# Kernel optimization log

Measured on AMD Instinct MI355X. Metric: run time of the kernel, lower is better.

The kernel has to match this reference:

```python
import jax, jax.numpy as jnp
import numpy as np

K_SEM = 5          # max_semantic_edges
THRESH = 0.2       # semantic_threshold
NEG_INF = -1e30


def setup_inputs() -> dict:
    key = jax.random.key(0)
    k1, k2 = jax.random.split(key)
    message_embeddings = jax.random.normal(k1, (8192, 256), dtype=jnp.float32)
    edge_emb_table = jax.random.normal(k2, (2, 64), dtype=jnp.float32)
    return {"message_embeddings": message_embeddings, "edge_emb_table": edge_emb_table}


def reference(message_embeddings, edge_emb_table):
    N = message_embeddings.shape[0]

    # ---- temporal edges: for each i -> [i,i+1] then [i+1,i] (interleaved) ----
    i = jnp.arange(N - 1)
    fwd = jnp.stack([i, i + 1])            # [2, N-1]
    bwd = jnp.stack([i + 1, i])            # [2, N-1]
    temporal = jnp.stack([fwd, bwd], axis=2).reshape(2, -1)   # [2, 2(N-1)]
    n_temporal = 2 * (N - 1)

    # ---- semantic edges: per-row top-k over sim[i, :i] with threshold ----
    norm = jnp.sqrt(jnp.sum(message_embeddings * message_embeddings, axis=1, keepdims=True))
    emb_n = message_embeddings / jnp.maximum(norm, 1e-12)     # F.normalize(p=2)
    sim = emb_n @ emb_n.T                                      # [N, N]

    r = jnp.arange(N)[:, None]
    c = jnp.arange(N)[None, :]
    # zero out diagonal and adjacent (temporal) pairs, as the torch mask does
    sim = sim * (jnp.abs(r - c) > 1)
    # restrict candidates to j < i (strictly earlier messages)
    cand = jnp.where(c < r, sim, NEG_INF)                      # [N, N]

    vals, idxs = jax.lax.top_k(cand, K_SEM)                    # [N, K]
    sem_src = idxs.reshape(-1)                                 # [N*K]
    sem_dst = jnp.repeat(jnp.arange(N), K_SEM)                 # [N*K]
    sem_valid = (vals > THRESH).reshape(-1)                    # [N*K]

    # ---- assemble padded fixed-size edge set ----
    edge_index = jnp.concatenate([temporal, jnp.stack([sem_src, sem_dst])], axis=1)
    edge_types = jnp.concatenate(
        [jnp.zeros((n_temporal,), jnp.int32), jnp.ones((N * K_SEM,), jnp.int32)])
    valid = jnp.concatenate([jnp.ones((n_temporal,), bool), sem_valid])

    edge_attr = edge_emb_table[edge_types] * valid[:, None].astype(edge_emb_table.dtype)
    edge_index = jnp.where(valid[None, :], edge_index, -1)
    return edge_index, edge_attr, valid
```

## Files before the change

kernel.cpp:

```cpp
#include <hip/hip_runtime.h>

#define N_MSG 8192
#define DIM 256
#define KS 5
#define THRESH 0.2f
#define QSCALE 192.0f
#define FILT_I 6672
#define N_TEMPORAL (2*(N_MSG-1))
#define N_EDGES (N_TEMPORAL + N_MSG*KS)
#define ATTR_OFF (2*N_EDGES)
#define VALID_OFF (ATTR_OFF + N_EDGES*64)
#define BM 128
#define NTILE (N_MSG / BM)
#define NBLOCKS (NTILE*(NTILE+1)/2)
#define CAP 32

typedef int   i32x4 __attribute__((ext_vector_type(4)));

__device__ __forceinline__ void gload_lds16(const void* g, void* l) {
    __builtin_amdgcn_global_load_lds(
        (const __attribute__((address_space(1))) void*)g,
        (__attribute__((address_space(3))) void*)l, 16, 0, 0);
}

__device__ __forceinline__ void ins5(float v, int j, float (&vv)[KS], int (&xx)[KS]) {
    float cv = v; int cj = j;
#pragma unroll
    for (int k = 0; k < KS; ++k) {
        bool b = (cv > vv[k]) || (cv == vv[k] && cj < xx[k]);
        float tv = b ? vv[k] : cv; int tj = b ? xx[k] : cj;
        vv[k] = b ? cv : vv[k];    xx[k] = b ? cj : xx[k];
        cv = tv; cj = tj;
    }
}

__global__ void normalize_k(const float* __restrict__ emb, float* __restrict__ embn,
                            unsigned int* __restrict__ embq, int* __restrict__ cnt) {
    int lane = threadIdx.x & 63;
    int row = blockIdx.x * 4 + (threadIdx.x >> 6);
    const float4 x = *(const float4*)(emb + (size_t)row * DIM + lane * 4);
    float ss = x.x * x.x;
    ss = fmaf(x.y, x.y, ss); ss = fmaf(x.z, x.z, ss); ss = fmaf(x.w, x.w, ss);
#pragma unroll
    for (int off = 1; off <= 32; off <<= 1) ss += __shfl_xor(ss, off);
    float nrm = fmaxf(sqrtf(ss), 1e-12f);
    float4 y; y.x = x.x / nrm; y.y = x.y / nrm; y.z = x.z / nrm; y.w = x.w / nrm;
    *(float4*)(embn + (size_t)row * DIM + lane * 4) = y;
    int q0 = (int)rintf(fminf(fmaxf(y.x * QSCALE, -127.f), 127.f));
    int q1 = (int)rintf(fminf(fmaxf(y.y * QSCALE, -127.f), 127.f));
    int q2 = (int)rintf(fminf(fmaxf(y.z * QSCALE, -127.f), 127.f));
    int q3 = (int)rintf(fminf(fmaxf(y.w * QSCALE, -127.f), 127.f));
    embq[(size_t)row * 64 + lane] =
        (q0 & 255) | ((q1 & 255) << 8) | ((q2 & 255) << 16) | ((q3 & 255) << 24);
    if (lane == 0) cnt[row] = 0;
}

__global__ __launch_bounds__(256, 4)
void sim_filter_k(const signed char* __restrict__ embq, int* __restrict__ cnt,
                  int* __restrict__ cidx) {
    __shared__ __align__(16) signed char Aq[2][BM * 64];
    __shared__ __align__(16) signed char Bq[2][BM * 64];

    int t = blockIdx.x;
    int bi = (int)((sqrtf(8.0f * (float)t + 1.0f) - 1.0f) * 0.5f);
    while ((bi + 1) * (bi + 2) / 2 <= t) ++bi;
    while (bi * (bi + 1) / 2 > t) --bi;
    int bj = t - bi * (bi + 1) / 2;
    const int i0 = bi * BM, j0 = bj * BM;

    const int tid = threadIdx.x;
    const int lane = tid & 63;
    const int ws = tid >> 6;
    const int wm = ws >> 1, wn = ws & 1;
    const int lr = lane & 15, kb = lane >> 4;

    const int gm = tid & 127;
    const int gk1 = tid >> 7, gk2 = gk1 + 2;

    const signed char* rowA = embq + (size_t)(i0 + gm) * DIM;
    const signed char* rowB = embq + (size_t)(j0 + gm) * DIM;

    auto stage = [&](int step, int buf) {
        gload_lds16(rowA + step * 64 + gk1 * 16, &Aq[buf][(size_t)tid * 16]);
        gload_lds16(rowA + step * 64 + gk2 * 16, &Aq[buf][((size_t)tid + 256) * 16]);
        gload_lds16(rowB + step * 64 + gk1 * 16, &Bq[buf][(size_t)tid * 16]);
        gload_lds16(rowB + step * 64 + gk2 * 16, &Bq[buf][((size_t)tid + 256) * 16]);
        asm volatile("" ::: "memory");
    };

    i32x4 acc[4][4];
#pragma unroll
    for (int m = 0; m < 4; ++m)
#pragma unroll
        for (int n = 0; n < 4; ++n) { i32x4 z = {0, 0, 0, 0}; acc[m][n] = z; }

    auto compute = [&](int slot) {
        i32x4 a[4], b[4];
#pragma unroll
        for (int f = 0; f < 4; ++f) {
            a[f] = *(const i32x4*)&Aq[slot][(size_t)(kb * 128 + wm * 64 + f * 16 + lr) * 16];
            b[f] = *(const i32x4*)&Bq[slot][(size_t)(kb * 128 + wn * 64 + f * 16 + lr) * 16];
        }
#pragma unroll
        for (int m = 0; m < 4; ++m)
#pragma unroll
            for (int n = 0; n < 4; ++n)
                acc[m][n] = __builtin_amdgcn_mfma_i32_16x16x64_i8(a[m], b[n], acc[m][n], 0, 0, 0);
    };

    stage(0, 0);
#pragma unroll
    for (int tk = 0; tk < 4; ++tk) {
        const int cur = tk & 1;
        if (tk < 3) {
            stage(tk + 1, cur ^ 1);
            asm volatile("s_waitcnt vmcnt(4)" ::: "memory");
        } else {
            asm volatile("s_waitcnt vmcnt(0)" ::: "memory");
        }
        __builtin_amdgcn_s_barrier();
        __builtin_amdgcn_sched_barrier(0);
        compute(cur);
        if (tk < 3) {
            __builtin_amdgcn_sched_barrier(0);
            __builtin_amdgcn_s_barrier();
        }
    }

#pragma unroll
    for (int m = 0; m < 4; ++m) {
        int i = i0 + wm * 64 + m * 16 + kb * 4;
#pragma unroll
        for (int n = 0; n < 4; ++n) {
            int j = j0 + wn * 64 + n * 16 + lr;
#pragma unroll
            for (int r = 0; r < 4; ++r) {
                int v = acc[m][n][r];
                int ii = i + r;
                if (v > FILT_I && j <= ii - 2) {
                    int c = atomicAdd(&cnt[ii], 1);
                    if (c < CAP) cidx[(size_t)ii * CAP + c] = j;
                }
            }
        }
    }
}

template<bool FUSE>
__global__ void rescue_k(const float* __restrict__ embn, const int* __restrict__ cnt,
                         const int* __restrict__ cidx, const float* __restrict__ table,
                         float* __restrict__ out) {
    int lane = threadIdx.x & 63;
    int i = blockIdx.x * 4 + (threadIdx.x >> 6);
    int nc = cnt[i]; if (nc > CAP) nc = CAP;

    float fv[KS]; int fx[KS];
#pragma unroll
    for (int k = 0; k < KS; ++k) { fv[k] = -1e30f; fx[k] = -1; }

    if (nc > 0) {
        const float4 a = *(const float4*)(embn + (size_t)i * DIM + lane * 4);
        for (int c = 0; c < nc; ++c) {
            int j = cidx[(size_t)i * CAP + c];
            const float4 b = *(const float4*)(embn + (size_t)j * DIM + lane * 4);
            float p = a.x * b.x;
            p = fmaf(a.y, b.y, p); p = fmaf(a.z, b.z, p); p = fmaf(a.w, b.w, p);
#pragma unroll
            for (int off = 1; off <= 32; off <<= 1) p += __shfl_xor(p, off);
            if (p > THRESH) ins5(p, j, fv, fx);
        }
    }
    int vcnt = 0;
#pragma unroll
    for (int k = 0; k < KS; ++k) vcnt += (fv[k] > THRESH) ? 1 : 0;

    float tsem = FUSE ? table[64 + lane] : 0.0f;
#pragma unroll
    for (int k = 0; k < KS; ++k) {
        int e = N_TEMPORAL + i * KS + k;
        bool val = (k < vcnt);
        if (lane == 0) {
            out[e]             = val ? (float)fx[k] : -1.0f;
            out[N_EDGES + e]   = val ? (float)i     : -1.0f;
            out[VALID_OFF + e] = val ? 1.0f : 0.0f;
        }
        if (FUSE) out[ATTR_OFF + (size_t)e * 64 + lane] = val ? tsem : 0.0f;
    }
    if (FUSE) {
        if (i < N_MSG - 1) {
            float ttem = table[lane];
            int e0 = 2 * i;
            out[ATTR_OFF + (size_t)e0 * 64 + lane]       = ttem;
            out[ATTR_OFF + (size_t)(e0 + 1) * 64 + lane] = ttem;
            if (lane == 0) {
                out[e0]                 = (float)i;
                out[N_EDGES + e0]       = (float)(i + 1);
                out[VALID_OFF + e0]     = 1.0f;
                out[e0 + 1]             = (float)(i + 1);
                out[N_EDGES + e0 + 1]   = (float)i;
                out[VALID_OFF + e0 + 1] = 1.0f;
            }
        }
    }
}

__global__ void attr_out_k(const float* __restrict__ table, float* __restrict__ out) {
    int idx = blockIdx.x * 256 + threadIdx.x;
    int e = idx >> 4, sub = idx & 15;
    if (e >= N_EDGES) return;
    float4 a4;
    if (e < N_TEMPORAL) {
        a4 = *(const float4*)(table + sub * 4);
        if (sub == 0) {
            int i = e >> 1;
            out[e]             = (e & 1) ? (float)(i + 1) : (float)i;
            out[N_EDGES + e]   = (e & 1) ? (float)i       : (float)(i + 1);
            out[VALID_OFF + e] = 1.0f;
        }
    } else {
        float vld = out[VALID_OFF + e];
        a4 = *(const float4*)(table + 64 + sub * 4);
        a4.x *= vld; a4.y *= vld; a4.z *= vld; a4.w *= vld;
    }
    *(float4*)(out + ATTR_OFF + (size_t)e * 64 + sub * 4) = a4;
}

extern "C" void kernel_launch(void* const* d_in, const int* in_sizes, int n_in,
                              void* d_out, int out_size, void* d_ws, size_t ws_size,
                              hipStream_t stream) {
    const float* emb   = (const float*)d_in[0];
    const float* table = (const float*)d_in[1];
    float* out = (float*)d_out;

    size_t embn_f  = (size_t)N_MSG * DIM;
    size_t embq_f  = (size_t)N_MSG * DIM / 4;
    size_t cidx_f  = (size_t)N_MSG * CAP;
    size_t cnt_f   = N_MSG;
    size_t need_bytes = (embn_f + embq_f + cidx_f + cnt_f) * 4;

    bool have_ws = (ws_size >= need_bytes);
    float* scratch = have_ws ? (float*)d_ws
                             : out + ATTR_OFF;
    float*        embn = scratch;
    unsigned int* embq = (unsigned int*)(scratch + embn_f);
    int*          cidx = (int*)(scratch + embn_f + embq_f);
    int*          cnt  = (int*)(scratch + embn_f + embq_f + cidx_f);

    normalize_k<<<N_MSG / 4, 256, 0, stream>>>(emb, embn, embq, cnt);
    sim_filter_k<<<NBLOCKS, 256, 0, stream>>>((const signed char*)embq, cnt, cidx);
    if (have_ws) {
        rescue_k<true><<<N_MSG / 4, 256, 0, stream>>>(embn, cnt, cidx, table, out);
    } else {
        rescue_k<false><<<N_MSG / 4, 256, 0, stream>>>(embn, cnt, cidx, table, out);
        attr_out_k<<<((size_t)N_EDGES * 16 + 255) / 256, 256, 0, stream>>>(table, out);
    }
}
```

Measured before the change: 71.62 us.

## Store quantized embeddings in MFMA-fragment layout and load directly to registers

The normalize kernel now writes the int8 quantized embeddings in a transposed, chunked layout where each 16-byte K-chunk of every row is contiguous across rows. The similarity kernel then loads MFMA operand fragments straight from global memory into registers, removing the LDS staging, double buffering and barriers. This drops LDS traffic and sync costs, but operand reuse now relies on L1/L2 caching instead of shared memory, and the loads are no longer explicitly overlapped with compute.

```diff
diff --git a/kernel.cpp b/kernel.cpp
--- a/kernel.cpp
+++ b/kernel.cpp
@@ -15,13 +15,7 @@
 #define NBLOCKS (NTILE*(NTILE+1)/2)
 #define CAP 32
 
-typedef int   i32x4 __attribute__((ext_vector_type(4)));
-
-__device__ __forceinline__ void gload_lds16(const void* g, void* l) {
-    __builtin_amdgcn_global_load_lds(
-        (const __attribute__((address_space(1))) void*)g,
-        (__attribute__((address_space(3))) void*)l, 16, 0, 0);
-}
+typedef int i32x4 __attribute__((ext_vector_type(4)));
 
 __device__ __forceinline__ void ins5(float v, int j, float (&vv)[KS], int (&xx)[KS]) {
     float cv = v; int cj = j;
@@ -35,7 +29,7 @@
 }
 
 __global__ void normalize_k(const float* __restrict__ emb, float* __restrict__ embn,
-                            unsigned int* __restrict__ embq, int* __restrict__ cnt) {
+                            unsigned int* __restrict__ embqT, int* __restrict__ cnt) {
     int lane = threadIdx.x & 63;
     int row = blockIdx.x * 4 + (threadIdx.x >> 6);
     const float4 x = *(const float4*)(emb + (size_t)row * DIM + lane * 4);
@@ -50,17 +44,15 @@
     int q1 = (int)rintf(fminf(fmaxf(y.y * QSCALE, -127.f), 127.f));
     int q2 = (int)rintf(fminf(fmaxf(y.z * QSCALE, -127.f), 127.f));
     int q3 = (int)rintf(fminf(fmaxf(y.w * QSCALE, -127.f), 127.f));
-    embq[(size_t)row * 64 + lane] =
+    unsigned int packed =
         (q0 & 255) | ((q1 & 255) << 8) | ((q2 & 255) << 16) | ((q3 & 255) << 24);
+    embqT[(((size_t)(lane >> 2) * N_MSG + row) << 2) | (lane & 3)] = packed;
     if (lane == 0) cnt[row] = 0;
 }
 
 __global__ __launch_bounds__(256, 4)
-void sim_filter_k(const signed char* __restrict__ embq, int* __restrict__ cnt,
+void sim_filter_k(const i32x4* __restrict__ T, int* __restrict__ cnt,
                   int* __restrict__ cidx) {
-    __shared__ __align__(16) signed char Aq[2][BM * 64];
-    __shared__ __align__(16) signed char Bq[2][BM * 64];
-
     int t = blockIdx.x;
     int bi = (int)((sqrtf(8.0f * (float)t + 1.0f) - 1.0f) * 0.5f);
     while ((bi + 1) * (bi + 2) / 2 <= t) ++bi;
@@ -74,57 +66,26 @@
     const int wm = ws >> 1, wn = ws & 1;
     const int lr = lane & 15, kb = lane >> 4;
 
-    const int gm = tid & 127;
-    const int gk1 = tid >> 7, gk2 = gk1 + 2;
-
-    const signed char* rowA = embq + (size_t)(i0 + gm) * DIM;
-    const signed char* rowB = embq + (size_t)(j0 + gm) * DIM;
-
-    auto stage = [&](int step, int buf) {
-        gload_lds16(rowA + step * 64 + gk1 * 16, &Aq[buf][(size_t)tid * 16]);
-        gload_lds16(rowA + step * 64 + gk2 * 16, &Aq[buf][((size_t)tid + 256) * 16]);
-        gload_lds16(rowB + step * 64 + gk1 * 16, &Bq[buf][(size_t)tid * 16]);
-        gload_lds16(rowB + step * 64 + gk2 * 16, &Bq[buf][((size_t)tid + 256) * 16]);
-        asm volatile("" ::: "memory");
-    };
-
     i32x4 acc[4][4];
 #pragma unroll
     for (int m = 0; m < 4; ++m)
 #pragma unroll
         for (int n = 0; n < 4; ++n) { i32x4 z = {0, 0, 0, 0}; acc[m][n] = z; }
 
-    auto compute = [&](int slot) {
+#pragma unroll
+    for (int kc = 0; kc < 4; ++kc) {
+        const i32x4* Tc = T + (size_t)(kc * 4 + kb) * N_MSG;
         i32x4 a[4], b[4];
 #pragma unroll
         for (int f = 0; f < 4; ++f) {
-            a[f] = *(const i32x4*)&Aq[slot][(size_t)(kb * 128 + wm * 64 + f * 16 + lr) * 16];
-            b[f] = *(const i32x4*)&Bq[slot][(size_t)(kb * 128 + wn * 64 + f * 16 + lr) * 16];
+            a[f] = Tc[i0 + wm * 64 + f * 16 + lr];
+            b[f] = Tc[j0 + wn * 64 + f * 16 + lr];
         }
 #pragma unroll
         for (int m = 0; m < 4; ++m)
 #pragma unroll
             for (int n = 0; n < 4; ++n)
                 acc[m][n] = __builtin_amdgcn_mfma_i32_16x16x64_i8(a[m], b[n], acc[m][n], 0, 0, 0);
-    };
-
-    stage(0, 0);
-#pragma unroll
-    for (int tk = 0; tk < 4; ++tk) {
-        const int cur = tk & 1;
-        if (tk < 3) {
-            stage(tk + 1, cur ^ 1);
-            asm volatile("s_waitcnt vmcnt(4)" ::: "memory");
-        } else {
-            asm volatile("s_waitcnt vmcnt(0)" ::: "memory");
-        }
-        __builtin_amdgcn_s_barrier();
-        __builtin_amdgcn_sched_barrier(0);
-        compute(cur);
-        if (tk < 3) {
-            __builtin_amdgcn_sched_barrier(0);
-            __builtin_amdgcn_s_barrier();
-        }
     }
 
 #pragma unroll
@@ -241,13 +202,13 @@
     bool have_ws = (ws_size >= need_bytes);
     float* scratch = have_ws ? (float*)d_ws
                              : out + ATTR_OFF;
-    float*        embn = scratch;
-    unsigned int* embq = (unsigned int*)(scratch + embn_f);
-    int*          cidx = (int*)(scratch + embn_f + embq_f);
-    int*          cnt  = (int*)(scratch + embn_f + embq_f + cidx_f);
-
-    normalize_k<<<N_MSG / 4, 256, 0, stream>>>(emb, embn, embq, cnt);
-    sim_filter_k<<<NBLOCKS, 256, 0, stream>>>((const signed char*)embq, cnt, cidx);
+    float*        embn  = scratch;
+    unsigned int* embqT = (unsigned int*)(scratch + embn_f);
+    int*          cidx  = (int*)(scratch + embn_f + embq_f);
+    int*          cnt   = (int*)(scratch + embn_f + embq_f + cidx_f);
+
+    normalize_k<<<N_MSG / 4, 256, 0, stream>>>(emb, embn, embqT, cnt);
+    sim_filter_k<<<NBLOCKS, 256, 0, stream>>>((const i32x4*)embqT, cnt, cidx);
     if (have_ws) {
         rescue_k<true><<<N_MSG / 4, 256, 0, stream>>>(embn, cnt, cidx, table, out);
     } else {
```

New measurement: 62.83 us. -12.3%, faster.
